# Kernel tuning notes

Measured on AMD Instinct MI355X. Metric: run time of the kernel, lower is better.

## Reference

```python
import jax, jax.numpy as jnp
import numpy as np


def _conv1x1_relu(x, w, b):
    # x: [B,C,T,H,W], w: [O,C], b: [O] -> 1x1x1 conv + ReLU
    y = jnp.einsum('oc,bcthw->bothw', w, x) + b[None, :, None, None, None]
    return jax.nn.relu(y)


def _maxpool3d_2(x):
    # MaxPool3d(kernel=2, stride=2, padding=0) over T,H,W
    return jax.lax.reduce_window(
        x, -jnp.inf, jax.lax.max,
        window_dimensions=(1, 1, 2, 2, 2),
        window_strides=(1, 1, 2, 2, 2),
        padding='VALID')


def setup_inputs() -> dict:
    key = jax.random.key(0)
    ks = jax.random.split(key, 10)
    B, C, T, H, W = 4, 128, 16, 32, 32
    C1, C2 = 4, 2
    d1, d2 = C // C1, C // C2  # 32, 64
    s = 0.05
    return {
        'x':  jax.random.normal(ks[0], (B, C, T, H, W), dtype=jnp.float32),
        'wf': jax.random.normal(ks[1], (d1, C), dtype=jnp.float32) * s,
        'bf': jnp.zeros((d1,), dtype=jnp.float32),
        'wg': jax.random.normal(ks[2], (d1, C), dtype=jnp.float32) * s,
        'bg': jnp.zeros((d1,), dtype=jnp.float32),
        'wh': jax.random.normal(ks[3], (d2, C), dtype=jnp.float32) * s,
        'bh': jnp.zeros((d2,), dtype=jnp.float32),
        'wo': jax.random.normal(ks[4], (C, d2), dtype=jnp.float32) * s,
        'bo': jnp.zeros((C,), dtype=jnp.float32),
        'gamma': jnp.asarray([0.5], dtype=jnp.float32),
    }


def reference(x, wf, bf, wg, bg, wh, bh, wo, bo, gamma):
    B, C, T, H, W = x.shape
    N = T * H * W
    theta = _conv1x1_relu(x, wf, bf).reshape(B, wf.shape[0], N)          # [B,d1,N]
    phi = _maxpool3d_2(_conv1x1_relu(x, wg, bg)).reshape(B, wg.shape[0], N // 8)  # [B,d1,M]
    g = _maxpool3d_2(_conv1x1_relu(x, wh, bh)).reshape(B, wh.shape[0], N // 8)    # [B,d2,M]
    # attn = softmax(theta^T @ phi) over keys (no 1/sqrt(d) scaling, as in source)
    scores = jnp.einsum('bcn,bcm->bnm', theta, phi)                      # [B,N,M]
    attn = jax.nn.softmax(scores, axis=-1)
    attn_g = jnp.einsum('bcm,bnm->bcn', g, attn).reshape(B, wh.shape[0], T, H, W)
    out = x + gamma[0] * _conv1x1_relu(attn_g, wo, bo)
    return out
```

## Files before the change

### kernel.cpp

```cpp
#include <hip/hip_runtime.h>
#include <hip/hip_bf16.h>

#define NB 4
#define NC 128
#define NN 16384
#define NM 2048

typedef __attribute__((ext_vector_type(8))) short bf16x8;
typedef __attribute__((ext_vector_type(4))) float f32x4;
typedef __attribute__((ext_vector_type(4))) unsigned short u16x4;
typedef __attribute__((ext_vector_type(2))) unsigned int u32x2;

#define MFMA16(a,b,c) __builtin_amdgcn_mfma_f32_16x16x32_bf16((a),(b),(c),0,0,0)

__device__ __forceinline__ unsigned short f2bf(float f){
  unsigned int u = __float_as_uint(f);
  u += 0x7fffu + ((u >> 16) & 1u);
  return (unsigned short)(u >> 16);
}
__device__ __forceinline__ float bf2f(unsigned short h){
  return __uint_as_float(((unsigned int)h) << 16);
}
__device__ __forceinline__ unsigned int packbf2(float lo, float hi){
  return (__float_as_uint(hi) & 0xffff0000u) | (__float_as_uint(lo) >> 16);
}

__global__ void k0_prep(const float* __restrict__ wf, const float* __restrict__ wg,
                        const float* __restrict__ wh, const float* __restrict__ bfp,
                        const float* __restrict__ bgp, const float* __restrict__ bhp,
                        const float* __restrict__ wo,
                        unsigned short* __restrict__ Wcat, unsigned short* __restrict__ wob,
                        float* __restrict__ bcat){
  int i = blockIdx.x * 256 + threadIdx.x;
  if (i < 16384){
    int o = i >> 7, c = i & 127;
    float v = (o < 32) ? wf[o*128 + c] : (o < 64) ? wg[(o-32)*128 + c] : wh[(o-64)*128 + c];
    Wcat[i] = f2bf(v);
  } else if (i < 24576){
    wob[i - 16384] = f2bf(wo[i - 16384]);
  } else if (i < 24704){
    int k = i - 24576;
    bcat[k] = (k < 32) ? bfp[k] : (k < 64) ? bgp[k-32] : bhp[k-64];
  }
}

__global__ void k1_transpose(const float* __restrict__ x, unsigned short* __restrict__ xT){
  __shared__ float tile[32][33];
  int bx = blockIdx.x;
  int nb = bx & 511, cb = (bx >> 9) & 3, b = bx >> 11;
  int t = threadIdx.x;
  int row = t >> 3, col4 = (t & 7) * 4;
  const float4 v = *(const float4*)(x + ((size_t)(b*128 + cb*32 + row)) * NN + nb*32 + col4);
  tile[row][col4+0] = v.x; tile[row][col4+1] = v.y;
  tile[row][col4+2] = v.z; tile[row][col4+3] = v.w;
  __syncthreads();
  int n = t >> 3, cv = (t & 7) * 4;
  u16x4 o;
  o[0] = f2bf(tile[cv+0][n]); o[1] = f2bf(tile[cv+1][n]);
  o[2] = f2bf(tile[cv+2][n]); o[3] = f2bf(tile[cv+3][n]);
  *(u16x4*)(xT + ((size_t)(b*NN + nb*32 + n)) * 128 + cb*32 + cv) = o;
}

__global__ __launch_bounds__(256, 2) void k2_conv(
    const unsigned short* __restrict__ xT, const unsigned short* __restrict__ Wcat,
    const float* __restrict__ bcat,
    unsigned short* __restrict__ thetaT, unsigned short* __restrict__ Yp){
  int blk = blockIdx.x;
  int b = blk >> 8, nblk = blk & 255;
  int tid = threadIdx.x;
  int lane = tid & 63, w = tid >> 6;
  int ln = lane & 15, gq = lane >> 4;
  int n = nblk*64 + w*16 + ln;
  const unsigned short* xrow = xT + ((size_t)b*NN + n) * 128;
  bf16x8 xf[4];
  #pragma unroll
  for (int kf = 0; kf < 4; ++kf)
    xf[kf] = *(const bf16x8*)(xrow + kf*32 + gq*8);
  #pragma unroll
  for (int ot = 0; ot < 8; ++ot){
    f32x4 acc = {0.f,0.f,0.f,0.f};
    #pragma unroll
    for (int kf = 0; kf < 4; ++kf){
      bf16x8 wfr = *(const bf16x8*)(Wcat + (ot*16 + ln)*128 + kf*32 + gq*8);
      acc = MFMA16(wfr, xf[kf], acc);
    }
    float y[4];
    #pragma unroll
    for (int i = 0; i < 4; ++i){
      int o = ot*16 + gq*4 + i;
      float v = acc[i] + bcat[o];
      y[i] = v > 0.f ? v : 0.f;
    }
    if (ot < 2){
      u16x4 pk;
      #pragma unroll
      for (int i = 0; i < 4; ++i) pk[i] = f2bf(y[i]);
      *(u16x4*)(thetaT + ((size_t)b*NN + n)*32 + ot*16 + gq*4) = pk;
    } else {
      #pragma unroll
      for (int i = 0; i < 4; ++i){
        float ym = fmaxf(y[i], __shfl_xor(y[i], 1));
        if ((ln & 1) == 0){
          int r = ot*16 + gq*4 + i - 32;
          Yp[((size_t)b*96 + r)*8192 + (n >> 1)] = f2bf(ym);
        }
      }
    }
  }
}

__global__ void k3_pool(const unsigned short* __restrict__ Yp,
                        unsigned short* __restrict__ phiT, unsigned short* __restrict__ g_){
  int i = blockIdx.x*256 + threadIdx.x;
  if (i < 262144){
    int c = i & 31, m = (i >> 5) & 2047, b = i >> 16;
    int tq = m >> 8, hq = (m >> 4) & 15, wq = m & 15;
    size_t base = ((size_t)b*96 + c)*8192 + tq*1024 + hq*32 + wq;
    float v0 = bf2f(Yp[base]),     v1 = bf2f(Yp[base+16]);
    float v2 = bf2f(Yp[base+512]), v3 = bf2f(Yp[base+528]);
    phiT[((size_t)b*NM + m)*32 + c] = f2bf(fmaxf(fmaxf(v0,v1), fmaxf(v2,v3)));
  } else if (i < 262144 + 524288){
    int j = i - 262144;
    int m = j & 2047, c2 = (j >> 11) & 63, b = j >> 17;
    int tq = m >> 8, hq = (m >> 4) & 15, wq = m & 15;
    size_t base = ((size_t)b*96 + 32 + c2)*8192 + tq*1024 + hq*32 + wq;
    float v0 = bf2f(Yp[base]),     v1 = bf2f(Yp[base+16]);
    float v2 = bf2f(Yp[base+512]), v3 = bf2f(Yp[base+528]);
    g_[((size_t)b*64 + c2)*NM + m] = f2bf(fmaxf(fmaxf(v0,v1), fmaxf(v2,v3)));
  }
}

__global__ __launch_bounds__(256, 2) void k4_attn(
    const unsigned short* __restrict__ thetaT, const unsigned short* __restrict__ phiT,
    const unsigned short* __restrict__ g_, unsigned short* __restrict__ attn_gT){
  __shared__ __align__(16) unsigned short phi_lds[2][32][40];
  __shared__ __align__(16) unsigned short g_lds[2][64][40];
  __shared__ __align__(16) unsigned short P_lds[4][16][40];

  int b = blockIdx.x >> 7, qb = blockIdx.x & 127;
  int tid = threadIdx.x;
  int lane = tid & 63, wv = tid >> 6;
  int ln = lane & 15, gq = lane >> 4;
  int nq = qb*128 + wv*32;

  const unsigned short* thb = thetaT + (size_t)b*NN*32;
  const unsigned short* phb = phiT   + (size_t)b*NM*32;
  const unsigned short* gb  = g_     + (size_t)b*64*NM;

  bf16x8 thf0 = *(const bf16x8*)(thb + (size_t)(nq + ln)*32 + gq*8);
  bf16x8 thf1 = *(const bf16x8*)(thb + (size_t)(nq + 16 + ln)*32 + gq*8);

  f32x4 acc[2][4];
  #pragma unroll
  for (int q = 0; q < 2; ++q)
    #pragma unroll
    for (int c2t = 0; c2t < 4; ++c2t) acc[q][c2t] = (f32x4){0.f,0.f,0.f,0.f};
  float lsum0 = 0.f, lsum1 = 0.f;

  int gr = tid >> 2, gp = tid & 3;
  const unsigned short* sgp_g = gb + (size_t)gr*NM + gp*8;
  unsigned short* slg0 = &g_lds[0][gr][gp*8];
  unsigned short* slg1 = &g_lds[1][gr][gp*8];
  bool hasphi = tid < 128;
  int pr = (tid >> 2) & 31, pp = tid & 3;
  const unsigned short* sgp_p = phb + pr*32 + pp*8;
  unsigned short* slp0 = &phi_lds[0][pr][pp*8];
  unsigned short* slp1 = &phi_lds[1][pr][pp*8];

  { bf16x8 srg = *(const bf16x8*)(sgp_g); *(bf16x8*)slg0 = srg; }
  if (hasphi){ bf16x8 srp = *(const bf16x8*)(sgp_p); *(bf16x8*)slp0 = srp; }
  __syncthreads();

  bf16x8 srg_n = {}, srp_n = {};
  for (int ch = 0; ch < 64; ++ch){
    int cur = ch & 1;
    if (ch + 1 < 64){
      srg_n = *(const bf16x8*)(sgp_g + (size_t)(ch+1)*32);
      if (hasphi) srp_n = *(const bf16x8*)(sgp_p + (size_t)(ch+1)*1024);
    }
    bf16x8 pf0 = *(const bf16x8*)(&phi_lds[cur][ln][gq*8]);
    bf16x8 pf1 = *(const bf16x8*)(&phi_lds[cur][16+ln][gq*8]);
    bf16x8 gf0 = *(const bf16x8*)(&g_lds[cur][ln][gq*8]);
    bf16x8 gf1 = *(const bf16x8*)(&g_lds[cur][16+ln][gq*8]);
    bf16x8 gf2 = *(const bf16x8*)(&g_lds[cur][32+ln][gq*8]);
    bf16x8 gf3 = *(const bf16x8*)(&g_lds[cur][48+ln][gq*8]);
    f32x4 z = {0.f,0.f,0.f,0.f};

    {
      f32x4 s0 = MFMA16(pf0, thf0, z);
      f32x4 s1 = MFMA16(pf1, thf0, z);
      float p0[4], p1[4];
      #pragma unroll
      for (int i = 0; i < 4; ++i){ p0[i] = __expf(s0[i]); p1[i] = __expf(s1[i]); }
      lsum0 += ((p0[0]+p0[1]) + (p0[2]+p0[3])) + ((p1[0]+p1[1]) + (p1[2]+p1[3]));
      u32x2 w0 = { packbf2(p0[0],p0[1]), packbf2(p0[2],p0[3]) };
      u32x2 w1 = { packbf2(p1[0],p1[1]), packbf2(p1[2],p1[3]) };
      *(u32x2*)(&P_lds[wv][ln][gq*4])      = w0;
      *(u32x2*)(&P_lds[wv][ln][16+gq*4])   = w1;
      bf16x8 paf = *(const bf16x8*)(&P_lds[wv][ln][gq*8]);
      acc[0][0] = MFMA16(paf, gf0, acc[0][0]);
      acc[0][1] = MFMA16(paf, gf1, acc[0][1]);
      acc[0][2] = MFMA16(paf, gf2, acc[0][2]);
      acc[0][3] = MFMA16(paf, gf3, acc[0][3]);
    }
    {
      f32x4 s0 = MFMA16(pf0, thf1, z);
      f32x4 s1 = MFMA16(pf1, thf1, z);
      float p0[4], p1[4];
      #pragma unroll
      for (int i = 0; i < 4; ++i){ p0[i] = __expf(s0[i]); p1[i] = __expf(s1[i]); }
      lsum1 += ((p0[0]+p0[1]) + (p0[2]+p0[3])) + ((p1[0]+p1[1]) + (p1[2]+p1[3]));
      u32x2 w0 = { packbf2(p0[0],p0[1]), packbf2(p0[2],p0[3]) };
      u32x2 w1 = { packbf2(p1[0],p1[1]), packbf2(p1[2],p1[3]) };
      *(u32x2*)(&P_lds[wv][ln][gq*4])      = w0;
      *(u32x2*)(&P_lds[wv][ln][16+gq*4])   = w1;
      bf16x8 paf = *(const bf16x8*)(&P_lds[wv][ln][gq*8]);
      acc[1][0] = MFMA16(paf, gf0, acc[1][0]);
      acc[1][1] = MFMA16(paf, gf1, acc[1][1]);
      acc[1][2] = MFMA16(paf, gf2, acc[1][2]);
      acc[1][3] = MFMA16(paf, gf3, acc[1][3]);
    }
    if (ch + 1 < 64){
      *(bf16x8*)(((ch+1)&1) ? slg1 : slg0) = srg_n;
      if (hasphi) *(bf16x8*)(((ch+1)&1) ? slp1 : slp0) = srp_n;
    }
    __syncthreads();
  }

  lsum0 += __shfl_xor(lsum0, 16); lsum0 += __shfl_xor(lsum0, 32);
  lsum1 += __shfl_xor(lsum1, 16); lsum1 += __shfl_xor(lsum1, 32);

  unsigned short* agb = attn_gT + (size_t)b*NN*64;
  #pragma unroll
  for (int i = 0; i < 4; ++i){
    float li0 = 1.0f / __shfl(lsum0, gq*4 + i);
    float li1 = 1.0f / __shfl(lsum1, gq*4 + i);
    int r0 = nq + gq*4 + i, r1 = nq + 16 + gq*4 + i;
    #pragma unroll
    for (int c2t = 0; c2t < 4; ++c2t){
      agb[(size_t)r0*64 + c2t*16 + ln] = f2bf(acc[0][c2t][i] * li0);
      agb[(size_t)r1*64 + c2t*16 + ln] = f2bf(acc[1][c2t][i] * li1);
    }
  }
}

__global__ __launch_bounds__(256, 2) void k5_out(
    const float* __restrict__ x, const unsigned short* __restrict__ attn_gT,
    const unsigned short* __restrict__ wob, const float* __restrict__ bo,
    const float* __restrict__ gamma, float* __restrict__ out){
  int blk = blockIdx.x;
  int b = blk >> 8, nblk = blk & 255;
  int tid = threadIdx.x;
  int lane = tid & 63, w = tid >> 6;
  int ln = lane & 15, gq = lane >> 4;
  int n = nblk*64 + w*16 + ln;
  const unsigned short* ag = attn_gT + ((size_t)b*NN + n)*64;
  bf16x8 bfr0 = *(const bf16x8*)(ag + gq*8);
  bf16x8 bfr1 = *(const bf16x8*)(ag + 32 + gq*8);
  float gam = gamma[0];
  #pragma unroll
  for (int ot = 0; ot < 8; ++ot){
    f32x4 acc = {0.f,0.f,0.f,0.f};
    bf16x8 a0 = *(const bf16x8*)(wob + (ot*16 + ln)*64 + gq*8);
    bf16x8 a1 = *(const bf16x8*)(wob + (ot*16 + ln)*64 + 32 + gq*8);
    acc = MFMA16(a0, bfr0, acc);
    acc = MFMA16(a1, bfr1, acc);
    #pragma unroll
    for (int i = 0; i < 4; ++i){
      int o = ot*16 + gq*4 + i;
      size_t idx = ((size_t)b*128 + o)*NN + n;
      float v = acc[i] + bo[o];
      v = v > 0.f ? v : 0.f;
      out[idx] = x[idx] + gam * v;
    }
  }
}

extern "C" void kernel_launch(void* const* d_in, const int* in_sizes, int n_in,
                              void* d_out, int out_size, void* d_ws, size_t ws_size,
                              hipStream_t stream){
  const float* x   = (const float*)d_in[0];
  const float* wf  = (const float*)d_in[1];
  const float* bfp = (const float*)d_in[2];
  const float* wg  = (const float*)d_in[3];
  const float* bgp = (const float*)d_in[4];
  const float* wh  = (const float*)d_in[5];
  const float* bhp = (const float*)d_in[6];
  const float* wo  = (const float*)d_in[7];
  const float* bo  = (const float*)d_in[8];
  const float* gam = (const float*)d_in[9];
  float* out = (float*)d_out;
  char* ws = (char*)d_ws;

  const size_t OFF_WCAT = 0;
  const size_t OFF_WO   = 32768;
  const size_t OFF_BCAT = 49152;
  const size_t OFF_XT   = 65536;
  const size_t OFF_TH   = OFF_XT + (size_t)NB*NN*128*2;
  const size_t OFF_YP   = OFF_TH + (size_t)NB*NN*32*2;
  const size_t OFF_PHI  = OFF_YP + (size_t)NB*96*8192*2;
  const size_t OFF_G    = OFF_PHI + (size_t)NB*NM*32*2;

  unsigned short* Wcat    = (unsigned short*)(ws + OFF_WCAT);
  unsigned short* wob     = (unsigned short*)(ws + OFF_WO);
  float*          bcat    = (float*)(ws + OFF_BCAT);
  unsigned short* xT      = (unsigned short*)(ws + OFF_XT);
  unsigned short* thetaT  = (unsigned short*)(ws + OFF_TH);
  unsigned short* Yp      = (unsigned short*)(ws + OFF_YP);
  unsigned short* phiT    = (unsigned short*)(ws + OFF_PHI);
  unsigned short* g_      = (unsigned short*)(ws + OFF_G);
  unsigned short* attn_gT = xT;

  k0_prep<<<97, 256, 0, stream>>>(wf, wg, wh, bfp, bgp, bhp, wo, Wcat, wob, bcat);
  k1_transpose<<<8192, 256, 0, stream>>>(x, xT);
  k2_conv<<<1024, 256, 0, stream>>>(xT, Wcat, bcat, thetaT, Yp);
  k3_pool<<<3072, 256, 0, stream>>>(Yp, phiT, g_);
  k4_attn<<<512, 256, 0, stream>>>(thetaT, phiT, g_, attn_gT);
  k5_out<<<1024, 256, 0, stream>>>(x, attn_gT, wob, bo, gam, out);
}
```

Baseline: 184.1 us.

## Fuse transpose into conv, pool W/H in-kernel, split attention keys in two

Drops the separate transpose kernel. The conv kernel now loads fp32 x directly, converts it to bf16 and transposes it through LDS. It also does the W and H max-pooling in LDS before writing a reduced intermediate, so the pool kernel only reduces over T and has far less traffic. Attention is split into two key halves per query block, doubling the grid, and unnormalized partial accumulators and row sums are written to global memory. The output kernel merges the two halves and normalizes them. Because the split has no running max, it relies on the existing softmax handling, and it adds extra global traffic for the partials.

```diff
diff --git a/kernel.cpp b/kernel.cpp
--- a/kernel.cpp
+++ b/kernel.cpp
@@ -44,38 +44,40 @@
   }
 }
 
-__global__ void k1_transpose(const float* __restrict__ x, unsigned short* __restrict__ xT){
-  __shared__ float tile[32][33];
-  int bx = blockIdx.x;
-  int nb = bx & 511, cb = (bx >> 9) & 3, b = bx >> 11;
-  int t = threadIdx.x;
-  int row = t >> 3, col4 = (t & 7) * 4;
-  const float4 v = *(const float4*)(x + ((size_t)(b*128 + cb*32 + row)) * NN + nb*32 + col4);
-  tile[row][col4+0] = v.x; tile[row][col4+1] = v.y;
-  tile[row][col4+2] = v.z; tile[row][col4+3] = v.w;
-  __syncthreads();
-  int n = t >> 3, cv = (t & 7) * 4;
-  u16x4 o;
-  o[0] = f2bf(tile[cv+0][n]); o[1] = f2bf(tile[cv+1][n]);
-  o[2] = f2bf(tile[cv+2][n]); o[3] = f2bf(tile[cv+3][n]);
-  *(u16x4*)(xT + ((size_t)(b*NN + nb*32 + n)) * 128 + cb*32 + cv) = o;
-}
-
-__global__ __launch_bounds__(256, 2) void k2_conv(
-    const unsigned short* __restrict__ xT, const unsigned short* __restrict__ Wcat,
+__global__ __launch_bounds__(256, 4) void k2_conv(
+    const float* __restrict__ x, const unsigned short* __restrict__ Wcat,
     const float* __restrict__ bcat,
-    unsigned short* __restrict__ thetaT, unsigned short* __restrict__ Yp){
+    unsigned short* __restrict__ thetaT, unsigned short* __restrict__ Ywh){
+  __shared__ __align__(16) unsigned short xtile[64][132];
+  __shared__ unsigned short Ytmp[96][33];
   int blk = blockIdx.x;
   int b = blk >> 8, nblk = blk & 255;
+  int n0 = nblk * 64;
   int tid = threadIdx.x;
+
+  {
+    int c = tid >> 1, half = tid & 1;
+    const float* xr = x + ((size_t)(b*128 + c)) * NN + n0 + half*32;
+    #pragma unroll
+    for (int j = 0; j < 8; ++j){
+      float4 v = *(const float4*)(xr + j*4);
+      int nl = half*32 + j*4;
+      xtile[nl+0][c] = f2bf(v.x);
+      xtile[nl+1][c] = f2bf(v.y);
+      xtile[nl+2][c] = f2bf(v.z);
+      xtile[nl+3][c] = f2bf(v.w);
+    }
+  }
+  __syncthreads();
+
   int lane = tid & 63, w = tid >> 6;
   int ln = lane & 15, gq = lane >> 4;
-  int n = nblk*64 + w*16 + ln;
-  const unsigned short* xrow = xT + ((size_t)b*NN + n) * 128;
+  int n = n0 + w*16 + ln;
   bf16x8 xf[4];
   #pragma unroll
   for (int kf = 0; kf < 4; ++kf)
-    xf[kf] = *(const bf16x8*)(xrow + kf*32 + gq*8);
+    xf[kf] = *(const bf16x8*)(&xtile[w*16 + ln][kf*32 + gq*8]);
+
   #pragma unroll
   for (int ot = 0; ot < 8; ++ot){
     f32x4 acc = {0.f,0.f,0.f,0.f};
@@ -102,46 +104,83 @@
         float ym = fmaxf(y[i], __shfl_xor(y[i], 1));
         if ((ln & 1) == 0){
           int r = ot*16 + gq*4 + i - 32;
-          Yp[((size_t)b*96 + r)*8192 + (n >> 1)] = f2bf(ym);
+          Ytmp[r][(w*16 + ln) >> 1] = f2bf(ym);
         }
       }
     }
   }
-}
-
-__global__ void k3_pool(const unsigned short* __restrict__ Yp,
+  __syncthreads();
+
+  int tt = n0 >> 10;
+  int h2 = nblk & 15;
+  #pragma unroll
+  for (int q = 0; q < 6; ++q){
+    int idx = q*256 + tid;
+    int r = idx >> 4, j = idx & 15;
+    unsigned short a = Ytmp[r][j], bsh = Ytmp[r][j+16];
+    unsigned short v = a > bsh ? a : bsh;
+    Ywh[(((size_t)(b*96 + r))*16 + tt)*256 + h2*16 + j] = v;
+  }
+}
+
+__global__ void k3_pool(const unsigned short* __restrict__ Ywh,
                         unsigned short* __restrict__ phiT, unsigned short* __restrict__ g_){
-  int i = blockIdx.x*256 + threadIdx.x;
-  if (i < 262144){
-    int c = i & 31, m = (i >> 5) & 2047, b = i >> 16;
-    int tq = m >> 8, hq = (m >> 4) & 15, wq = m & 15;
-    size_t base = ((size_t)b*96 + c)*8192 + tq*1024 + hq*32 + wq;
-    float v0 = bf2f(Yp[base]),     v1 = bf2f(Yp[base+16]);
-    float v2 = bf2f(Yp[base+512]), v3 = bf2f(Yp[base+528]);
-    phiT[((size_t)b*NM + m)*32 + c] = f2bf(fmaxf(fmaxf(v0,v1), fmaxf(v2,v3)));
-  } else if (i < 262144 + 524288){
-    int j = i - 262144;
-    int m = j & 2047, c2 = (j >> 11) & 63, b = j >> 17;
-    int tq = m >> 8, hq = (m >> 4) & 15, wq = m & 15;
-    size_t base = ((size_t)b*96 + 32 + c2)*8192 + tq*1024 + hq*32 + wq;
-    float v0 = bf2f(Yp[base]),     v1 = bf2f(Yp[base+16]);
-    float v2 = bf2f(Yp[base+512]), v3 = bf2f(Yp[base+528]);
-    g_[((size_t)b*64 + c2)*NM + m] = f2bf(fmaxf(fmaxf(v0,v1), fmaxf(v2,v3)));
-  }
-}
-
-__global__ __launch_bounds__(256, 2) void k4_attn(
+  __shared__ unsigned short trans[64][36];
+  int blk = blockIdx.x;
+  int t = threadIdx.x;
+  if (blk < 128){
+    int b = blk >> 5, mseg = blk & 31;
+    int m0 = mseg * 64;
+    int u = m0 >> 8, p0 = m0 & 255;
+    int c = t >> 3, mj = t & 7;
+    const unsigned short* r0 = Ywh + (((size_t)(b*96 + c))*16 + 2*u)*256 + p0 + mj*8;
+    const unsigned short* r1 = r0 + 256;
+    #pragma unroll
+    for (int k = 0; k < 8; ++k){
+      unsigned short a = r0[k], bsh = r1[k];
+      trans[mj*8 + k][c] = a > bsh ? a : bsh;
+    }
+    __syncthreads();
+    int ml = t >> 2, cg = t & 3;
+    u16x4 o0, o1;
+    #pragma unroll
+    for (int k = 0; k < 4; ++k){ o0[k] = trans[ml][cg*8 + k]; o1[k] = trans[ml][cg*8 + 4 + k]; }
+    *(u16x4*)(phiT + ((size_t)b*NM + m0 + ml)*32 + cg*8)     = o0;
+    *(u16x4*)(phiT + ((size_t)b*NM + m0 + ml)*32 + cg*8 + 4) = o1;
+  } else {
+    int blk2 = blk - 128;
+    int b = blk2 >> 6, c2 = blk2 & 63;
+    int u = t >> 5, p = (t & 31) * 8;
+    const unsigned short* r0 = Ywh + (((size_t)(b*96 + 32 + c2))*16 + 2*u)*256 + p;
+    const unsigned short* r1 = r0 + 256;
+    u16x4 o0, o1;
+    #pragma unroll
+    for (int k = 0; k < 4; ++k){
+      unsigned short a0 = r0[k],   b0 = r1[k];
+      unsigned short a1 = r0[4+k], b1 = r1[4+k];
+      o0[k] = a0 > b0 ? a0 : b0;
+      o1[k] = a1 > b1 ? a1 : b1;
+    }
+    *(u16x4*)(g_ + ((size_t)(b*64 + c2))*NM + t*8)     = o0;
+    *(u16x4*)(g_ + ((size_t)(b*64 + c2))*NM + t*8 + 4) = o1;
+  }
+}
+
+__global__ __launch_bounds__(256, 4) void k4_attn(
     const unsigned short* __restrict__ thetaT, const unsigned short* __restrict__ phiT,
-    const unsigned short* __restrict__ g_, unsigned short* __restrict__ attn_gT){
+    const unsigned short* __restrict__ g_, unsigned short* __restrict__ pacc,
+    float* __restrict__ lsumA){
   __shared__ __align__(16) unsigned short phi_lds[2][32][40];
   __shared__ __align__(16) unsigned short g_lds[2][64][40];
   __shared__ __align__(16) unsigned short P_lds[4][16][40];
 
-  int b = blockIdx.x >> 7, qb = blockIdx.x & 127;
+  int bx = blockIdx.x;
+  int b = bx >> 8, qb = (bx >> 1) & 127, kh = bx & 1;
   int tid = threadIdx.x;
   int lane = tid & 63, wv = tid >> 6;
   int ln = lane & 15, gq = lane >> 4;
   int nq = qb*128 + wv*32;
+  int ch0 = kh * 32;
 
   const unsigned short* thb = thetaT + (size_t)b*NN*32;
   const unsigned short* phb = phiT   + (size_t)b*NM*32;
@@ -158,12 +197,12 @@
   float lsum0 = 0.f, lsum1 = 0.f;
 
   int gr = tid >> 2, gp = tid & 3;
-  const unsigned short* sgp_g = gb + (size_t)gr*NM + gp*8;
+  const unsigned short* sgp_g = gb + (size_t)gr*NM + ch0*32 + gp*8;
   unsigned short* slg0 = &g_lds[0][gr][gp*8];
   unsigned short* slg1 = &g_lds[1][gr][gp*8];
   bool hasphi = tid < 128;
   int pr = (tid >> 2) & 31, pp = tid & 3;
-  const unsigned short* sgp_p = phb + pr*32 + pp*8;
+  const unsigned short* sgp_p = phb + ((size_t)(ch0*32 + pr))*32 + pp*8;
   unsigned short* slp0 = &phi_lds[0][pr][pp*8];
   unsigned short* slp1 = &phi_lds[1][pr][pp*8];
 
@@ -172,11 +211,11 @@
   __syncthreads();
 
   bf16x8 srg_n = {}, srp_n = {};
-  for (int ch = 0; ch < 64; ++ch){
-    int cur = ch & 1;
-    if (ch + 1 < 64){
-      srg_n = *(const bf16x8*)(sgp_g + (size_t)(ch+1)*32);
-      if (hasphi) srp_n = *(const bf16x8*)(sgp_p + (size_t)(ch+1)*1024);
+  for (int lc = 0; lc < 32; ++lc){
+    int cur = lc & 1;
+    if (lc + 1 < 32){
+      srg_n = *(const bf16x8*)(sgp_g + (size_t)(lc+1)*32);
+      if (hasphi) srp_n = *(const bf16x8*)(sgp_p + (size_t)(lc+1)*1024);
     }
     bf16x8 pf0 = *(const bf16x8*)(&phi_lds[cur][ln][gq*8]);
     bf16x8 pf1 = *(const bf16x8*)(&phi_lds[cur][16+ln][gq*8]);
@@ -220,9 +259,9 @@
       acc[1][2] = MFMA16(paf, gf2, acc[1][2]);
       acc[1][3] = MFMA16(paf, gf3, acc[1][3]);
     }
-    if (ch + 1 < 64){
-      *(bf16x8*)(((ch+1)&1) ? slg1 : slg0) = srg_n;
-      if (hasphi) *(bf16x8*)(((ch+1)&1) ? slp1 : slp0) = srp_n;
+    if (lc + 1 < 32){
+      *(bf16x8*)(((lc+1)&1) ? slg1 : slg0) = srg_n;
+      if (hasphi) *(bf16x8*)(((lc+1)&1) ? slp1 : slp0) = srp_n;
     }
     __syncthreads();
   }
@@ -230,22 +269,34 @@
   lsum0 += __shfl_xor(lsum0, 16); lsum0 += __shfl_xor(lsum0, 32);
   lsum1 += __shfl_xor(lsum1, 16); lsum1 += __shfl_xor(lsum1, 32);
 
-  unsigned short* agb = attn_gT + (size_t)b*NN*64;
+  unsigned short* pb = pacc + ((size_t)(kh*NB + b))*NN*64;
   #pragma unroll
   for (int i = 0; i < 4; ++i){
-    float li0 = 1.0f / __shfl(lsum0, gq*4 + i);
-    float li1 = 1.0f / __shfl(lsum1, gq*4 + i);
     int r0 = nq + gq*4 + i, r1 = nq + 16 + gq*4 + i;
     #pragma unroll
     for (int c2t = 0; c2t < 4; ++c2t){
-      agb[(size_t)r0*64 + c2t*16 + ln] = f2bf(acc[0][c2t][i] * li0);
-      agb[(size_t)r1*64 + c2t*16 + ln] = f2bf(acc[1][c2t][i] * li1);
-    }
-  }
-}
-
-__global__ __launch_bounds__(256, 2) void k5_out(
-    const float* __restrict__ x, const unsigned short* __restrict__ attn_gT,
+      pb[(size_t)r0*64 + c2t*16 + ln] = f2bf(acc[0][c2t][i]);
+      pb[(size_t)r1*64 + c2t*16 + ln] = f2bf(acc[1][c2t][i]);
+    }
+  }
+  size_t lbase = ((size_t)(kh*NB + b))*NN;
+  if (gq == 0)      lsumA[lbase + nq + ln]      = lsum0;
+  else if (gq == 1) lsumA[lbase + nq + 16 + ln] = lsum1;
+}
+
+__device__ __forceinline__ bf16x8 combine8(bf16x8 a, bf16x8 b, float inv){
+  bf16x8 r;
+  #pragma unroll
+  for (int k = 0; k < 8; ++k){
+    float f = (bf2f((unsigned short)a[k]) + bf2f((unsigned short)b[k])) * inv;
+    r[k] = (short)f2bf(f);
+  }
+  return r;
+}
+
+__global__ __launch_bounds__(256, 4) void k5_out(
+    const float* __restrict__ x, const unsigned short* __restrict__ pacc,
+    const float* __restrict__ lsumA,
     const unsigned short* __restrict__ wob, const float* __restrict__ bo,
     const float* __restrict__ gamma, float* __restrict__ out){
   int blk = blockIdx.x;
@@ -254,9 +305,18 @@
   int lane = tid & 63, w = tid >> 6;
   int ln = lane & 15, gq = lane >> 4;
   int n = nblk*64 + w*16 + ln;
-  const unsigned short* ag = attn_gT + ((size_t)b*NN + n)*64;
-  bf16x8 bfr0 = *(const bf16x8*)(ag + gq*8);
-  bf16x8 bfr1 = *(const bf16x8*)(ag + 32 + gq*8);
+
+  const unsigned short* p0 = pacc + ((size_t)b*NN + n)*64;
+  const unsigned short* p1 = pacc + ((size_t)(NB + b)*NN + n)*64;
+  float l = lsumA[(size_t)b*NN + n] + lsumA[(size_t)(NB + b)*NN + n];
+  float inv = 1.0f / l;
+  bf16x8 a0lo = *(const bf16x8*)(p0 + gq*8);
+  bf16x8 a1lo = *(const bf16x8*)(p1 + gq*8);
+  bf16x8 a0hi = *(const bf16x8*)(p0 + 32 + gq*8);
+  bf16x8 a1hi = *(const bf16x8*)(p1 + 32 + gq*8);
+  bf16x8 bfr0 = combine8(a0lo, a1lo, inv);
+  bf16x8 bfr1 = combine8(a0hi, a1hi, inv);
+
   float gam = gamma[0];
   #pragma unroll
   for (int ot = 0; ot < 8; ++ot){
@@ -295,26 +355,26 @@
   const size_t OFF_WCAT = 0;
   const size_t OFF_WO   = 32768;
   const size_t OFF_BCAT = 49152;
-  const size_t OFF_XT   = 65536;
-  const size_t OFF_TH   = OFF_XT + (size_t)NB*NN*128*2;
-  const size_t OFF_YP   = OFF_TH + (size_t)NB*NN*32*2;
-  const size_t OFF_PHI  = OFF_YP + (size_t)NB*96*8192*2;
+  const size_t OFF_TH   = 65536;
+  const size_t OFF_YWH  = OFF_TH  + (size_t)NB*NN*32*2;
+  const size_t OFF_PHI  = OFF_YWH + (size_t)NB*96*16*256*2;
   const size_t OFF_G    = OFF_PHI + (size_t)NB*NM*32*2;
+  const size_t OFF_PACC = OFF_G   + (size_t)NB*64*NM*2;
+  const size_t OFF_LSUM = OFF_PACC+ (size_t)2*NB*NN*64*2;
 
   unsigned short* Wcat    = (unsigned short*)(ws + OFF_WCAT);
   unsigned short* wob     = (unsigned short*)(ws + OFF_WO);
   float*          bcat    = (float*)(ws + OFF_BCAT);
-  unsigned short* xT      = (unsigned short*)(ws + OFF_XT);
   unsigned short* thetaT  = (unsigned short*)(ws + OFF_TH);
-  unsigned short* Yp      = (unsigned short*)(ws + OFF_YP);
+  unsigned short* Ywh     = (unsigned short*)(ws + OFF_YWH);
   unsigned short* phiT    = (unsigned short*)(ws + OFF_PHI);
   unsigned short* g_      = (unsigned short*)(ws + OFF_G);
-  unsigned short* attn_gT = xT;
+  unsigned short* pacc    = (unsigned short*)(ws + OFF_PACC);
+  float*          lsumA   = (float*)(ws + OFF_LSUM);
 
   k0_prep<<<97, 256, 0, stream>>>(wf, wg, wh, bfp, bgp, bhp, wo, Wcat, wob, bcat);
-  k1_transpose<<<8192, 256, 0, stream>>>(x, xT);
-  k2_conv<<<1024, 256, 0, stream>>>(xT, Wcat, bcat, thetaT, Yp);
-  k3_pool<<<3072, 256, 0, stream>>>(Yp, phiT, g_);
-  k4_attn<<<512, 256, 0, stream>>>(thetaT, phiT, g_, attn_gT);
-  k5_out<<<1024, 256, 0, stream>>>(x, attn_gT, wob, bo, gam, out);
-}
+  k2_conv<<<1024, 256, 0, stream>>>(x, Wcat, bcat, thetaT, Ywh);
+  k3_pool<<<384, 256, 0, stream>>>(Ywh, phiT, g_);
+  k4_attn<<<1024, 256, 0, stream>>>(thetaT, phiT, g_, pacc, lsumA);
+  k5_out<<<1024, 256, 0, stream>>>(x, pacc, lsumA, wob, bo, gam, out);
+}
```

After: 170.0 us. 1.08x faster.
